# Kernel optimization log

Measured on AMD Instinct MI355X. Metric: run time of the kernel, lower is better.

Reference implementation:

```python
import jax, jax.numpy as jnp
import numpy as np
from jax import lax

B, S, D_IN, D_OUT = 2, 1024, 2048, 2048
H, DK, DV, K = 8, 64, 128, 4
CONV_DIM = H * (3 * DK + DV)  # q,k,f each DK per head; v is DV per head
G = H * DV


def _rsa_scan(q, k, v, f, W):
    # q,k,f: [B,S,H,DK]; v: [B,S,H,DV]; W: [H,DV,DV]
    # matrix-valued per-head state St: [B,H,DK,DV], GRU-style gated update
    qs = jnp.moveaxis(q, 1, 0)
    ks = jnp.moveaxis(k, 1, 0)
    vs = jnp.moveaxis(v, 1, 0)
    fs = jnp.moveaxis(f, 1, 0)
    S0 = jnp.zeros((q.shape[0], H, DK, DV), q.dtype)

    def step(St, xs):
        qt, kt, vt, ft = xs
        g = jax.nn.sigmoid(ft)  # [B,H,DK] forget gate
        cand = jnp.tanh(vt[:, :, None, :] + jnp.einsum('bhkv,hvw->bhkw', St, W))
        St = g[..., None] * St + kt[..., None] * cand  # [B,H,DK,DV]
        yt = jnp.einsum('bhk,bhkv->bhv', qt, St)  # readout [B,H,DV]
        return St, yt

    _, ys = lax.scan(step, S0, (qs, ks, vs, fs))
    return jnp.moveaxis(ys, 0, 1)  # [B,S,H,DV]


def setup_inputs() -> dict:
    key = jax.random.key(0)
    ks = jax.random.split(key, 11)
    std = 0.02
    return {
        'x': jax.random.normal(ks[0], (B, S, D_IN), jnp.float32),
        'w_in': jax.random.normal(ks[1], (CONV_DIM + G, D_IN), jnp.float32) * std,
        'b_in': jax.random.normal(ks[2], (CONV_DIM + G,), jnp.float32) * std,
        'conv_w': jax.random.normal(ks[3], (CONV_DIM, 1, K), jnp.float32) * std,
        'conv_b': jax.random.normal(ks[4], (CONV_DIM,), jnp.float32) * std,
        'D': 1.0 + 0.1 * jax.random.normal(ks[5], (H, DV), jnp.float32),
        'state_weight': jax.random.normal(ks[6], (H, DV, DV), jnp.float32) * std,
        'forget_multiplier': 0.1 * jax.random.normal(ks[7], (H,), jnp.float32),
        'forget_bias': 0.1 * jax.random.normal(ks[8], (H, DK), jnp.float32),
        'g_w': 1.0 + 0.1 * jax.random.normal(ks[9], (G,), jnp.float32),
        'w_out': jax.random.normal(ks[10], (D_OUT, G), jnp.float32) * std,
    }


def reference(x, w_in, b_in, conv_w, conv_b, D, state_weight, forget_multiplier, forget_bias, g_w, w_out):
    h = x @ w_in.T + b_in  # input projection [B,S,CONV_DIM+G]
    conv_in, gate = h[..., :CONV_DIM], h[..., CONV_DIM:]
    # causal depthwise conv1d (left pad K-1) + SiLU activation
    xc = jnp.swapaxes(conv_in, 1, 2)  # [B,C,S]
    yc = lax.conv_general_dilated(xc, conv_w, (1,), [(K - 1, 0)], feature_group_count=CONV_DIM)
    yc = jax.nn.silu(yc + conv_b[None, :, None])
    yc = jnp.swapaxes(yc, 1, 2)  # [B,S,CONV_DIM]
    o = 0
    q = yc[..., o:o + H * DK].reshape(B, S, H, DK); o += H * DK
    k = yc[..., o:o + H * DK].reshape(B, S, H, DK); o += H * DK
    v = yc[..., o:o + H * DV].reshape(B, S, H, DV); o += H * DV
    f = yc[..., o:o + H * DK].reshape(B, S, H, DK)
    # p=2 key normalization over head dim (elementwise_affine=False)
    k = k * lax.rsqrt(jnp.sum(k * k, -1, keepdims=True) + 1e-12)
    f = 2.0 * jax.nn.sigmoid(forget_multiplier)[None, None, :, None] * (f + forget_bias[None, None])
    y = _rsa_scan(q, k, v, f, state_weight)  # [B,S,H,DV]
    y = (y + v * D[None, None]).reshape(B, S, G)
    y = y * jax.nn.silu(gate)
    y = y * lax.rsqrt(jnp.mean(y * y, -1, keepdims=True) + 1e-6) * g_w  # RMSNorm
    return y @ w_out.T
```

## Files before the change

### kernel.cpp

```cpp
#include <hip/hip_runtime.h>

typedef unsigned short u16;
typedef unsigned int u32;
typedef __attribute__((ext_vector_type(8))) short short8;
typedef __attribute__((ext_vector_type(4))) float f32x4;

#define N_B 2
#define N_S 1024
#define N_DIN 2048
#define N_DOUT 2048
#define N_H 8
#define N_DK 64
#define N_DV 128
#define N_CONVD 2560
#define N_G 1024
#define N_NH 3584

#define TANH_SCALE 2.8853901817f
#define INV_TANH_SCALE 0.34657359f

__device__ __forceinline__ u16 f2bf(float f) {
  u32 u = __float_as_uint(f);
  u32 r = (u + 0x7FFFu + ((u >> 16) & 1u)) >> 16;
  return (u16)r;
}
__device__ __forceinline__ float fsigmoid(float x) {
  return __builtin_amdgcn_rcpf(1.f + __builtin_amdgcn_exp2f(-1.44269504f * x));
}
__device__ __forceinline__ u32 pack_bf16_rhu(float a, float b) {
  u32 ua = __float_as_uint(a) + 0x8000u;
  u32 ub = __float_as_uint(b) + 0x8000u;
  return __builtin_amdgcn_perm(ub, ua, 0x07060302u);
}
__device__ __forceinline__ void gll16(const void* g, void* l) {
  __builtin_amdgcn_global_load_lds((const __attribute__((address_space(1))) u32*)g,
                                   (__attribute__((address_space(3))) u32*)l, 16, 0, 0);
}

__global__ void cvt_kernel(const float* __restrict__ src, u16* __restrict__ dst, int n) {
  int i4 = (blockIdx.x * 256 + threadIdx.x) * 4;
  if (i4 + 3 < n) {
    float4 v = *(const float4*)&src[i4];
    dst[i4 + 0] = f2bf(v.x);
    dst[i4 + 1] = f2bf(v.y);
    dst[i4 + 2] = f2bf(v.z);
    dst[i4 + 3] = f2bf(v.w);
  }
}

__global__ void wtprep_kernel(const float* __restrict__ sw, u16* __restrict__ wtb) {
  int idx = blockIdx.x * 256 + threadIdx.x;
  if (idx >= N_H * 128 * 128) return;
  int h = idx >> 14;
  int rem = idx & 16383;
  int j = rem >> 7, v = rem & 127;
  wtb[idx] = f2bf(TANH_SCALE * sw[((size_t)h * 128 + v) * 128 + j]);
}

__global__ __launch_bounds__(256, 2) void gemm_bt(const u16* __restrict__ A,
                                                  const u16* __restrict__ B,
                                                  const float* __restrict__ bias,
                                                  float* __restrict__ C, int M, int N, int K) {
  const int tid = threadIdx.x;
  const int lane = tid & 63, w = tid >> 6;
  const int u = lane >> 4, m16 = lane & 15;
  const int wm = w & 1, wn = w >> 1;
  const int m0 = blockIdx.y * 128, n0 = blockIdx.x * 128;

  __shared__ __align__(16) u16 As[128 * 32];
  __shared__ __align__(16) u16 Bs[128 * 32];

  f32x4 acc[4][4];
#pragma unroll
  for (int i = 0; i < 4; ++i)
#pragma unroll
    for (int j = 0; j < 4; ++j)
#pragma unroll
      for (int r = 0; r < 4; ++r) acc[i][j][r] = 0.f;

  const int row0 = tid >> 2, col0 = (tid & 3) * 8;
  for (int kk = 0; kk < K; kk += 32) {
#pragma unroll
    for (int q = 0; q < 2; ++q) {
      int chunk = tid + 256 * q;
      int row = row0 + 64 * q;
      gll16(&A[(size_t)(m0 + row) * K + kk + col0], &As[chunk * 8]);
      gll16(&B[(size_t)(n0 + row) * K + kk + col0], &Bs[chunk * 8]);
    }
    __syncthreads();
    short8 af[4], bfr[4];
#pragma unroll
    for (int i = 0; i < 4; ++i) af[i] = *(const short8*)&As[(64 * wm + 16 * i + m16) * 32 + 8 * u];
#pragma unroll
    for (int i = 0; i < 4; ++i) bfr[i] = *(const short8*)&Bs[(64 * wn + 16 * i + m16) * 32 + 8 * u];
#pragma unroll
    for (int am = 0; am < 4; ++am)
#pragma unroll
      for (int bn = 0; bn < 4; ++bn)
        acc[am][bn] = __builtin_amdgcn_mfma_f32_16x16x32_bf16(af[am], bfr[bn], acc[am][bn], 0, 0, 0);
    __syncthreads();
  }
#pragma unroll
  for (int am = 0; am < 4; ++am)
#pragma unroll
    for (int bn = 0; bn < 4; ++bn) {
      int n = n0 + 64 * wn + 16 * bn + m16;
      float bv = bias ? bias[n] : 0.f;
#pragma unroll
      for (int r = 0; r < 4; ++r) {
        int m = m0 + 64 * wm + 16 * am + 4 * u + r;
        C[(size_t)m * N + n] = acc[am][bn][r] + bv;
      }
    }
}

__global__ __launch_bounds__(320, 4) void conv_kernel(const float* __restrict__ h,
                                                      const float* __restrict__ cw,
                                                      const float* __restrict__ cb,
                                                      const float* __restrict__ fm,
                                                      const float* __restrict__ fb,
                                                      float* __restrict__ SCIN) {
  const int bid = blockIdx.x;
  const int t = bid & 1023, chain = bid >> 10;
  const int b = chain >> 3, hh = chain & 7;
  const int tid = threadIdx.x;

  int c, outoff;
  if (tid < 64) { c = hh * 64 + tid; outoff = tid * 4; }
  else if (tid < 128) { int i = tid - 64; c = 512 + hh * 64 + i; outoff = i * 4 + 1; }
  else if (tid < 192) { int i = tid - 128; c = 2048 + hh * 64 + i; outoff = i * 4 + 2; }
  else { int j = tid - 192; c = 1024 + hh * 128 + j; outoff = 256 + j; }

  float4 w4 = *(const float4*)&cw[c * 4];
  const float* wp = (const float*)&w4;
  float acc = cb[c];
  const float* hrow = h + ((size_t)(b * 1024 + t)) * N_NH + c;
#pragma unroll
  for (int j = 0; j < 4; ++j) {
    int tt = t - 3 + j;
    if (tt >= 0) acc += wp[j] * hrow[(ptrdiff_t)(j - 3) * N_NH];
  }
  float yv = acc * fsigmoid(acc);

  if (tid >= 64 && tid < 128) {
    float s = yv * yv;
#pragma unroll
    for (int m = 1; m < 64; m <<= 1) s += __shfl_xor(s, m, 64);
    yv *= __builtin_amdgcn_rsqf(s + 1e-12f);
  } else if (tid >= 128 && tid < 192) {
    float scale2 = 2.f * fsigmoid(fm[hh]);
    yv = fsigmoid(scale2 * (yv + fb[hh * 64 + (tid - 128)]));
  } else if (tid >= 192) {
    yv *= TANH_SCALE;
  }
  SCIN[(size_t)bid * 384 + outoff] = yv;
}

__global__ __launch_bounds__(512, 2) void scan_kernel(const u16* __restrict__ Wtb,
                                                      const float* __restrict__ SCIN,
                                                      float* __restrict__ Ybp) {
  const int tid = threadIdx.x;
  const int lane = tid & 63, wv = tid >> 6;
  const int u = lane >> 4, m16 = lane & 15;
  const int chain = blockIdx.x >> 2;
  const int ig = blockIdx.x & 3;
  const int hh = chain & 7;

  __shared__ __align__(16) u16 Slds[2][16 * 136];

  short8 Wfrag[4];
  {
    const u16* wb = Wtb + ((size_t)hh * 128 + (16 * wv + m16)) * 128 + 8 * u;
#pragma unroll
    for (int kc = 0; kc < 4; ++kc) Wfrag[kc] = *(const short8*)(wb + 32 * kc);
  }

  for (int x = tid; x < 2 * 16 * 136; x += 512) ((u16*)Slds)[x] = 0;

  const float* scin_c = SCIN + (size_t)chain * 1024 * 384;
  float* ybase = Ybp + ((size_t)(chain * 4 + ig)) * 1024 * 128;

  float Sreg[4] = {0.f, 0.f, 0.f, 0.f};

  float4 qkg = *(const float4*)&scin_c[(16 * ig + m16) * 4];
  float4 v4 = *(const float4*)&scin_c[256 + 16 * wv + 4 * u];

  __syncthreads();

  for (int t = 0; t < 1024; ++t) {
    const int tn = (t + 1) & 1023;
    const float* pn = scin_c + (size_t)tn * 384;
    float4 qkgn = *(const float4*)&pn[(16 * ig + m16) * 4];
    float4 vn = *(const float4*)&pn[256 + 16 * wv + 4 * u];

    const u16* Sr = Slds[t & 1];
    u16* Sw = Slds[(t + 1) & 1];

    short8 Bfrag[4];
#pragma unroll
    for (int kc = 0; kc < 4; ++kc)
      Bfrag[kc] = *(const short8*)&Sr[m16 * 136 + 32 * kc + 8 * u];

    f32x4 acc0, acc1 = {0.f, 0.f, 0.f, 0.f};
    acc0[0] = v4.x; acc0[1] = v4.y; acc0[2] = v4.z; acc0[3] = v4.w;
    acc0 = __builtin_amdgcn_mfma_f32_16x16x32_bf16(Wfrag[0], Bfrag[0], acc0, 0, 0, 0);
    acc1 = __builtin_amdgcn_mfma_f32_16x16x32_bf16(Wfrag[1], Bfrag[1], acc1, 0, 0, 0);
    acc0 = __builtin_amdgcn_mfma_f32_16x16x32_bf16(Wfrag[2], Bfrag[2], acc0, 0, 0, 0);
    acc1 = __builtin_amdgcn_mfma_f32_16x16x32_bf16(Wfrag[3], Bfrag[3], acc1, 0, 0, 0);

    const float qv = qkg.x, kv = qkg.y, gv = qkg.z;
    float p[4];
#pragma unroll
    for (int r = 0; r < 4; ++r) {
      float arg = acc0[r] + acc1[r];
      float e = __builtin_amdgcn_exp2f(arg);
      float cand = 1.f - 2.f * __builtin_amdgcn_rcpf(e + 1.f);
      Sreg[r] = gv * Sreg[r] + kv * cand;
      p[r] = qv * Sreg[r];
    }

    uint2 pck;
    pck.x = pack_bf16_rhu(Sreg[0], Sreg[1]);
    pck.y = pack_bf16_rhu(Sreg[2], Sreg[3]);
    *(uint2*)&Sw[m16 * 136 + 16 * wv + 4 * u] = pck;

#pragma unroll
    for (int r = 0; r < 4; ++r) {
      float pr = p[r];
      pr += __int_as_float(__builtin_amdgcn_update_dpp(0, __float_as_int(pr), 0x111, 0xF, 0xF, true));
      pr += __int_as_float(__builtin_amdgcn_update_dpp(0, __float_as_int(pr), 0x112, 0xF, 0xF, true));
      pr += __int_as_float(__builtin_amdgcn_update_dpp(0, __float_as_int(pr), 0x114, 0xF, 0xF, true));
      pr += __int_as_float(__builtin_amdgcn_update_dpp(0, __float_as_int(pr), 0x118, 0xF, 0xF, true));
      p[r] = pr;
    }
    if (m16 == 15) {
      f32x4 yo;
      yo[0] = p[0]; yo[1] = p[1]; yo[2] = p[2]; yo[3] = p[3];
      *(f32x4*)(ybase + (size_t)t * 128 + 16 * wv + 4 * u) = yo;
    }

    asm volatile("s_waitcnt lgkmcnt(0)\n\ts_barrier" ::: "memory");

    qkg = qkgn; v4 = vn;
  }
}

__global__ __launch_bounds__(256, 2) void post_kernel(const float* __restrict__ Ybp,
                                                      const float* __restrict__ SCIN,
                                                      const float* __restrict__ h,
                                                      const float* __restrict__ Dp,
                                                      const float* __restrict__ gwv,
                                                      u16* __restrict__ Zb) {
  const int bt = blockIdx.x;
  const int b = bt >> 10, t = bt & 1023;
  const int lane = threadIdx.x & 63, wvi = threadIdx.x >> 6;
  float z[4];
  float ss = 0.f;
#pragma unroll
  for (int c = 0; c < 4; ++c) {
    int j = threadIdx.x + 256 * c;
    int head = j >> 7, dv = j & 127;
    int chain = b * 8 + head;
    float y = 0.f;
#pragma unroll
    for (int igx = 0; igx < 4; ++igx)
      y += Ybp[(((size_t)(chain * 4 + igx)) * 1024 + t) * 128 + dv];
    float v = SCIN[((size_t)chain * 1024 + t) * 384 + 256 + dv];
    float gate = h[((size_t)(b * 1024 + t)) * N_NH + 2560 + j];
    float zz = (y + v * (Dp[j] * INV_TANH_SCALE)) * (gate * fsigmoid(gate));
    z[c] = zz;
    ss += zz * zz;
  }
#pragma unroll
  for (int m = 1; m < 64; m <<= 1) ss += __shfl_xor(ss, m, 64);
  __shared__ float red[4];
  if (lane == 0) red[wvi] = ss;
  __syncthreads();
  float tot = red[0] + red[1] + red[2] + red[3];
  float scale = __builtin_amdgcn_rsqf(tot * (1.f / 1024.f) + 1e-6f);
#pragma unroll
  for (int c = 0; c < 4; ++c) {
    int j = threadIdx.x + 256 * c;
    Zb[(size_t)(b * 1024 + t) * 1024 + j] = f2bf(z[c] * scale * gwv[j]);
  }
}

extern "C" void kernel_launch(void* const* d_in, const int* in_sizes, int n_in,
                              void* d_out, int out_size, void* d_ws, size_t ws_size,
                              hipStream_t stream) {
  const float* x    = (const float*)d_in[0];
  const float* w_in = (const float*)d_in[1];
  const float* b_in = (const float*)d_in[2];
  const float* cw   = (const float*)d_in[3];
  const float* cb   = (const float*)d_in[4];
  const float* Dp   = (const float*)d_in[5];
  const float* sw   = (const float*)d_in[6];
  const float* fm   = (const float*)d_in[7];
  const float* fb   = (const float*)d_in[8];
  const float* gwv  = (const float*)d_in[9];
  const float* wo   = (const float*)d_in[10];
  float* out = (float*)d_out;

  char* p = (char*)d_ws;
  auto alloc = [&](size_t bytes) {
    char* r = p;
    p += (bytes + 255) & ~(size_t)255;
    return r;
  };
  u16* xb    = (u16*)alloc((size_t)2048 * 2048 * 2);
  u16* wib   = (u16*)alloc((size_t)3584 * 2048 * 2);
  u16* wob   = (u16*)alloc((size_t)2048 * 1024 * 2);
  u16* wtb   = (u16*)alloc((size_t)8 * 128 * 128 * 2);
  float* hbf = (float*)alloc((size_t)2048 * 3584 * 4);
  float* scin= (float*)alloc((size_t)16 * 1024 * 384 * 4);
  float* ybp = (float*)alloc((size_t)64 * 1024 * 128 * 4);
  u16* zb    = (u16*)alloc((size_t)2048 * 1024 * 2);

  cvt_kernel<<<4096, 256, 0, stream>>>(x, xb, 2048 * 2048);
  cvt_kernel<<<7168, 256, 0, stream>>>(w_in, wib, 3584 * 2048);
  cvt_kernel<<<2048, 256, 0, stream>>>(wo, wob, 2048 * 1024);
  wtprep_kernel<<<512, 256, 0, stream>>>(sw, wtb);

  gemm_bt<<<dim3(3584 / 128, 2048 / 128), 256, 0, stream>>>(xb, wib, b_in, hbf, 2048, 3584, 2048);

  conv_kernel<<<16 * 1024, 320, 0, stream>>>(hbf, cw, cb, fm, fb, scin);

  scan_kernel<<<64, 512, 0, stream>>>(wtb, scin, ybp);

  post_kernel<<<2048, 256, 0, stream>>>(ybp, scin, hbf, Dp, gwv, zb);

  gemm_bt<<<dim3(2048 / 128, 2048 / 128), 256, 0, stream>>>(zb, wob, nullptr, out, 2048, 2048, 1024);
}
```

Measured before the change: 663.4 us.

## Defer scan readout reduction a step and XOR-swizzle state LDS layout

Moves the per-step readout DPP reduction and output store off the recurrence critical path by computing them one iteration later, where they can overlap with the next step's MFMAs. Replaces the padded LDS state buffer with an XOR-swizzled unpadded layout to avoid bank conflicts, and issues the state reads before the global prefetch. It also folds the tanh candidate update into two FMAs. This adds a loop epilogue and live registers for the deferred partial products.

```diff
diff --git a/kernel.cpp b/kernel.cpp
--- a/kernel.cpp
+++ b/kernel.cpp
@@ -36,6 +36,13 @@
   __builtin_amdgcn_global_load_lds((const __attribute__((address_space(1))) u32*)g,
                                    (__attribute__((address_space(3))) u32*)l, 16, 0, 0);
 }
+__device__ __forceinline__ float dpp_prefix16(float x) {
+  x += __int_as_float(__builtin_amdgcn_update_dpp(0, __float_as_int(x), 0x111, 0xF, 0xF, true));
+  x += __int_as_float(__builtin_amdgcn_update_dpp(0, __float_as_int(x), 0x112, 0xF, 0xF, true));
+  x += __int_as_float(__builtin_amdgcn_update_dpp(0, __float_as_int(x), 0x114, 0xF, 0xF, true));
+  x += __int_as_float(__builtin_amdgcn_update_dpp(0, __float_as_int(x), 0x118, 0xF, 0xF, true));
+  return x;
+}
 
 __global__ void cvt_kernel(const float* __restrict__ src, u16* __restrict__ dst, int n) {
   int i4 = (blockIdx.x * 256 + threadIdx.x) * 4;
@@ -166,7 +173,7 @@
   const int ig = blockIdx.x & 3;
   const int hh = chain & 7;
 
-  __shared__ __align__(16) u16 Slds[2][16 * 136];
+  __shared__ __align__(16) u16 Slds[2][16 * 128];
 
   short8 Wfrag[4];
   {
@@ -175,31 +182,51 @@
     for (int kc = 0; kc < 4; ++kc) Wfrag[kc] = *(const short8*)(wb + 32 * kc);
   }
 
-  for (int x = tid; x < 2 * 16 * 136; x += 512) ((u16*)Slds)[x] = 0;
+  for (int x = tid; x < 2048; x += 512) ((u32*)Slds)[x] = 0u;
+
+  const int xr = m16 & 7;
+  int rdoff[4];
+#pragma unroll
+  for (int kc = 0; kc < 4; ++kc) rdoff[kc] = m16 * 256 + (((4 * kc + u) ^ xr) << 4);
+  const int wroff = m16 * 256 + ((((wv << 1) + (u >> 1)) ^ xr) << 4) + ((u & 1) << 3);
 
   const float* scin_c = SCIN + (size_t)chain * 1024 * 384;
   float* ybase = Ybp + ((size_t)(chain * 4 + ig)) * 1024 * 128;
 
   float Sreg[4] = {0.f, 0.f, 0.f, 0.f};
+  float pp[4] = {0.f, 0.f, 0.f, 0.f};
 
   float4 qkg = *(const float4*)&scin_c[(16 * ig + m16) * 4];
   float4 v4 = *(const float4*)&scin_c[256 + 16 * wv + 4 * u];
 
   __syncthreads();
 
+  char* ldsbase = (char*)&Slds[0][0];
+
   for (int t = 0; t < 1024; ++t) {
+    const char* Sr = ldsbase + ((t & 1) << 12);
+    char* Sw = ldsbase + (((t + 1) & 1) << 12);
+
+    short8 Bfrag[4];
+#pragma unroll
+    for (int kc = 0; kc < 4; ++kc) Bfrag[kc] = *(const short8*)(Sr + rdoff[kc]);
+
     const int tn = (t + 1) & 1023;
     const float* pn = scin_c + (size_t)tn * 384;
     float4 qkgn = *(const float4*)&pn[(16 * ig + m16) * 4];
     float4 vn = *(const float4*)&pn[256 + 16 * wv + 4 * u];
 
-    const u16* Sr = Slds[t & 1];
-    u16* Sw = Slds[(t + 1) & 1];
-
-    short8 Bfrag[4];
-#pragma unroll
-    for (int kc = 0; kc < 4; ++kc)
-      Bfrag[kc] = *(const short8*)&Sr[m16 * 136 + 32 * kc + 8 * u];
+    if (t > 0) {
+      float y0 = dpp_prefix16(pp[0]);
+      float y1 = dpp_prefix16(pp[1]);
+      float y2 = dpp_prefix16(pp[2]);
+      float y3 = dpp_prefix16(pp[3]);
+      if (m16 == 15) {
+        f32x4 yo;
+        yo[0] = y0; yo[1] = y1; yo[2] = y2; yo[3] = y3;
+        *(f32x4*)(ybase + (size_t)(t - 1) * 128 + 16 * wv + 4 * u) = yo;
+      }
+    }
 
     f32x4 acc0, acc1 = {0.f, 0.f, 0.f, 0.f};
     acc0[0] = v4.x; acc0[1] = v4.y; acc0[2] = v4.z; acc0[3] = v4.w;
@@ -209,39 +236,39 @@
     acc1 = __builtin_amdgcn_mfma_f32_16x16x32_bf16(Wfrag[3], Bfrag[3], acc1, 0, 0, 0);
 
     const float qv = qkg.x, kv = qkg.y, gv = qkg.z;
-    float p[4];
+    const float k2 = -2.f * kv;
 #pragma unroll
     for (int r = 0; r < 4; ++r) {
       float arg = acc0[r] + acc1[r];
       float e = __builtin_amdgcn_exp2f(arg);
-      float cand = 1.f - 2.f * __builtin_amdgcn_rcpf(e + 1.f);
-      Sreg[r] = gv * Sreg[r] + kv * cand;
-      p[r] = qv * Sreg[r];
+      float rc = __builtin_amdgcn_rcpf(e + 1.f);
+      float base = __builtin_fmaf(gv, Sreg[r], kv);
+      Sreg[r] = __builtin_fmaf(k2, rc, base);
     }
 
     uint2 pck;
     pck.x = pack_bf16_rhu(Sreg[0], Sreg[1]);
     pck.y = pack_bf16_rhu(Sreg[2], Sreg[3]);
-    *(uint2*)&Sw[m16 * 136 + 16 * wv + 4 * u] = pck;
-
-#pragma unroll
-    for (int r = 0; r < 4; ++r) {
-      float pr = p[r];
-      pr += __int_as_float(__builtin_amdgcn_update_dpp(0, __float_as_int(pr), 0x111, 0xF, 0xF, true));
-      pr += __int_as_float(__builtin_amdgcn_update_dpp(0, __float_as_int(pr), 0x112, 0xF, 0xF, true));
-      pr += __int_as_float(__builtin_amdgcn_update_dpp(0, __float_as_int(pr), 0x114, 0xF, 0xF, true));
-      pr += __int_as_float(__builtin_amdgcn_update_dpp(0, __float_as_int(pr), 0x118, 0xF, 0xF, true));
-      p[r] = pr;
-    }
+    *(uint2*)(Sw + wroff) = pck;
+
+#pragma unroll
+    for (int r = 0; r < 4; ++r) pp[r] = qv * Sreg[r];
+
+    asm volatile("s_waitcnt lgkmcnt(0)\n\ts_barrier" ::: "memory");
+
+    qkg = qkgn; v4 = vn;
+  }
+
+  {
+    float y0 = dpp_prefix16(pp[0]);
+    float y1 = dpp_prefix16(pp[1]);
+    float y2 = dpp_prefix16(pp[2]);
+    float y3 = dpp_prefix16(pp[3]);
     if (m16 == 15) {
       f32x4 yo;
-      yo[0] = p[0]; yo[1] = p[1]; yo[2] = p[2]; yo[3] = p[3];
-      *(f32x4*)(ybase + (size_t)t * 128 + 16 * wv + 4 * u) = yo;
-    }
-
-    asm volatile("s_waitcnt lgkmcnt(0)\n\ts_barrier" ::: "memory");
-
-    qkg = qkgn; v4 = vn;
+      yo[0] = y0; yo[1] = y1; yo[2] = y2; yo[3] = y3;
+      *(f32x4*)(ybase + (size_t)1023 * 128 + 16 * wv + 4 * u) = yo;
+    }
   }
 }
 
```

New measurement: 762.8 us. 1.15x slower.

## Split scan DK rows across more blocks based on available workspace

Applied to the files above, without the earlier changes.

The scan kernel is templated on how many DK rows each block owns (V). With enough workspace, 256 or 128 blocks run instead of 64, and each block loads only V distinct q/k/g rows, zeroing q for padded lanes. The per-row update is also folded into FMAs. Post_kernel then sums a variable number of partial outputs. This aims to raise parallelism on the latency-bound sequential scan, at the cost of duplicated 128x128 recurrence work, more MFMA per useful row, and more partial-output traffic in post_kernel.

```diff
diff --git a/kernel.cpp b/kernel.cpp
--- a/kernel.cpp
+++ b/kernel.cpp
@@ -36,6 +36,13 @@
   __builtin_amdgcn_global_load_lds((const __attribute__((address_space(1))) u32*)g,
                                    (__attribute__((address_space(3))) u32*)l, 16, 0, 0);
 }
+__device__ __forceinline__ float dpp_prefix16(float x) {
+  x += __int_as_float(__builtin_amdgcn_update_dpp(0, __float_as_int(x), 0x111, 0xF, 0xF, true));
+  x += __int_as_float(__builtin_amdgcn_update_dpp(0, __float_as_int(x), 0x112, 0xF, 0xF, true));
+  x += __int_as_float(__builtin_amdgcn_update_dpp(0, __float_as_int(x), 0x114, 0xF, 0xF, true));
+  x += __int_as_float(__builtin_amdgcn_update_dpp(0, __float_as_int(x), 0x118, 0xF, 0xF, true));
+  return x;
+}
 
 __global__ void cvt_kernel(const float* __restrict__ src, u16* __restrict__ dst, int n) {
   int i4 = (blockIdx.x * 256 + threadIdx.x) * 4;
@@ -156,14 +163,16 @@
   SCIN[(size_t)bid * 384 + outoff] = yv;
 }
 
+template <int V>
 __global__ __launch_bounds__(512, 2) void scan_kernel(const u16* __restrict__ Wtb,
                                                       const float* __restrict__ SCIN,
                                                       float* __restrict__ Ybp) {
+  const int NIG = 64 / V;
   const int tid = threadIdx.x;
   const int lane = tid & 63, wv = tid >> 6;
   const int u = lane >> 4, m16 = lane & 15;
-  const int chain = blockIdx.x >> 2;
-  const int ig = blockIdx.x & 3;
+  const int chain = blockIdx.x / NIG;
+  const int ig = blockIdx.x - chain * NIG;
   const int hh = chain & 7;
 
   __shared__ __align__(16) u16 Slds[2][16 * 136];
@@ -178,11 +187,15 @@
   for (int x = tid; x < 2 * 16 * 136; x += 512) ((u16*)Slds)[x] = 0;
 
   const float* scin_c = SCIN + (size_t)chain * 1024 * 384;
-  float* ybase = Ybp + ((size_t)(chain * 4 + ig)) * 1024 * 128;
+  float* ybase = Ybp + ((size_t)(chain * NIG + ig)) * 1024 * 128;
+
+  const int iload = V * ig + (m16 < V ? m16 : V - 1);
+  const bool qzero = (V < 16) && (m16 >= V);
 
   float Sreg[4] = {0.f, 0.f, 0.f, 0.f};
 
-  float4 qkg = *(const float4*)&scin_c[(16 * ig + m16) * 4];
+  float4 qkg = *(const float4*)&scin_c[iload * 4];
+  if (qzero) qkg.x = 0.f;
   float4 v4 = *(const float4*)&scin_c[256 + 16 * wv + 4 * u];
 
   __syncthreads();
@@ -190,7 +203,7 @@
   for (int t = 0; t < 1024; ++t) {
     const int tn = (t + 1) & 1023;
     const float* pn = scin_c + (size_t)tn * 384;
-    float4 qkgn = *(const float4*)&pn[(16 * ig + m16) * 4];
+    float4 qkgn = *(const float4*)&pn[iload * 4];
     float4 vn = *(const float4*)&pn[256 + 16 * wv + 4 * u];
 
     const u16* Sr = Slds[t & 1];
@@ -209,13 +222,15 @@
     acc1 = __builtin_amdgcn_mfma_f32_16x16x32_bf16(Wfrag[3], Bfrag[3], acc1, 0, 0, 0);
 
     const float qv = qkg.x, kv = qkg.y, gv = qkg.z;
+    const float k2 = -2.f * kv;
     float p[4];
 #pragma unroll
     for (int r = 0; r < 4; ++r) {
       float arg = acc0[r] + acc1[r];
       float e = __builtin_amdgcn_exp2f(arg);
-      float cand = 1.f - 2.f * __builtin_amdgcn_rcpf(e + 1.f);
-      Sreg[r] = gv * Sreg[r] + kv * cand;
+      float rc = __builtin_amdgcn_rcpf(e + 1.f);
+      float base = __builtin_fmaf(gv, Sreg[r], kv);
+      Sreg[r] = __builtin_fmaf(k2, rc, base);
       p[r] = qv * Sreg[r];
     }
 
@@ -225,14 +240,7 @@
     *(uint2*)&Sw[m16 * 136 + 16 * wv + 4 * u] = pck;
 
 #pragma unroll
-    for (int r = 0; r < 4; ++r) {
-      float pr = p[r];
-      pr += __int_as_float(__builtin_amdgcn_update_dpp(0, __float_as_int(pr), 0x111, 0xF, 0xF, true));
-      pr += __int_as_float(__builtin_amdgcn_update_dpp(0, __float_as_int(pr), 0x112, 0xF, 0xF, true));
-      pr += __int_as_float(__builtin_amdgcn_update_dpp(0, __float_as_int(pr), 0x114, 0xF, 0xF, true));
-      pr += __int_as_float(__builtin_amdgcn_update_dpp(0, __float_as_int(pr), 0x118, 0xF, 0xF, true));
-      p[r] = pr;
-    }
+    for (int r = 0; r < 4; ++r) p[r] = dpp_prefix16(p[r]);
     if (m16 == 15) {
       f32x4 yo;
       yo[0] = p[0]; yo[1] = p[1]; yo[2] = p[2]; yo[3] = p[3];
@@ -241,7 +249,9 @@
 
     asm volatile("s_waitcnt lgkmcnt(0)\n\ts_barrier" ::: "memory");
 
-    qkg = qkgn; v4 = vn;
+    qkg = qkgn;
+    if (qzero) qkg.x = 0.f;
+    v4 = vn;
   }
 }
 
@@ -250,7 +260,7 @@
                                                       const float* __restrict__ h,
                                                       const float* __restrict__ Dp,
                                                       const float* __restrict__ gwv,
-                                                      u16* __restrict__ Zb) {
+                                                      u16* __restrict__ Zb, int nparts) {
   const int bt = blockIdx.x;
   const int b = bt >> 10, t = bt & 1023;
   const int lane = threadIdx.x & 63, wvi = threadIdx.x >> 6;
@@ -262,9 +272,8 @@
     int head = j >> 7, dv = j & 127;
     int chain = b * 8 + head;
     float y = 0.f;
-#pragma unroll
-    for (int igx = 0; igx < 4; ++igx)
-      y += Ybp[(((size_t)(chain * 4 + igx)) * 1024 + t) * 128 + dv];
+    for (int igx = 0; igx < nparts; ++igx)
+      y += Ybp[(((size_t)(chain * nparts + igx)) * 1024 + t) * 128 + dv];
     float v = SCIN[((size_t)chain * 1024 + t) * 384 + 256 + dv];
     float gate = h[((size_t)(b * 1024 + t)) * N_NH + 2560 + j];
     float zz = (y + v * (Dp[j] * INV_TANH_SCALE)) * (gate * fsigmoid(gate));
@@ -313,8 +322,15 @@
   u16* wtb   = (u16*)alloc((size_t)8 * 128 * 128 * 2);
   float* hbf = (float*)alloc((size_t)2048 * 3584 * 4);
   float* scin= (float*)alloc((size_t)16 * 1024 * 384 * 4);
-  float* ybp = (float*)alloc((size_t)64 * 1024 * 128 * 4);
   u16* zb    = (u16*)alloc((size_t)2048 * 1024 * 2);
+
+  size_t used = (size_t)(p - (char*)d_ws);
+  size_t avail = (ws_size > used) ? ws_size - used : 0;
+  const size_t per_part = (size_t)16 * 1024 * 128 * 4;
+  int nig = 4;
+  if (avail >= 16 * per_part) nig = 16;
+  else if (avail >= 8 * per_part) nig = 8;
+  float* ybp = (float*)alloc((size_t)nig * per_part);
 
   cvt_kernel<<<4096, 256, 0, stream>>>(x, xb, 2048 * 2048);
   cvt_kernel<<<7168, 256, 0, stream>>>(w_in, wib, 3584 * 2048);
@@ -325,9 +341,11 @@
 
   conv_kernel<<<16 * 1024, 320, 0, stream>>>(hbf, cw, cb, fm, fb, scin);
 
-  scan_kernel<<<64, 512, 0, stream>>>(wtb, scin, ybp);
-
-  post_kernel<<<2048, 256, 0, stream>>>(ybp, scin, hbf, Dp, gwv, zb);
+  if (nig == 16)      scan_kernel<4><<<16 * 16, 512, 0, stream>>>(wtb, scin, ybp);
+  else if (nig == 8)  scan_kernel<8><<<16 * 8, 512, 0, stream>>>(wtb, scin, ybp);
+  else                scan_kernel<16><<<16 * 4, 512, 0, stream>>>(wtb, scin, ybp);
+
+  post_kernel<<<2048, 256, 0, stream>>>(ybp, scin, hbf, Dp, gwv, zb, nig);
 
   gemm_bt<<<dim3(2048 / 128, 2048 / 128), 256, 0, stream>>>(zb, wob, nullptr, out, 2048, 2048, 1024);
 }
```

Result: slower. 703.3 us (+6.0%).

## Restructure scan so each 4-wave block handles two key-row groups

Applied to the files above, without the earlier changes.

The scan kernel now runs 32 blocks of 256 threads instead of 64 blocks of 512. Each block processes two 16-row key groups of a chain, and each wave owns 32 output columns using two W fragments. Barrier cost is shared across twice the work, and the two independent MFMA chains interleave to hide latency. In exchange, each wave runs a longer serial instruction sequence per timestep and only half as many CUs are used. The tanh update is also folded into fused FMAs.

```diff
diff --git a/kernel.cpp b/kernel.cpp
--- a/kernel.cpp
+++ b/kernel.cpp
@@ -36,6 +36,13 @@
   __builtin_amdgcn_global_load_lds((const __attribute__((address_space(1))) u32*)g,
                                    (__attribute__((address_space(3))) u32*)l, 16, 0, 0);
 }
+__device__ __forceinline__ float dpp_prefix16(float x) {
+  x += __int_as_float(__builtin_amdgcn_update_dpp(0, __float_as_int(x), 0x111, 0xF, 0xF, true));
+  x += __int_as_float(__builtin_amdgcn_update_dpp(0, __float_as_int(x), 0x112, 0xF, 0xF, true));
+  x += __int_as_float(__builtin_amdgcn_update_dpp(0, __float_as_int(x), 0x114, 0xF, 0xF, true));
+  x += __int_as_float(__builtin_amdgcn_update_dpp(0, __float_as_int(x), 0x118, 0xF, 0xF, true));
+  return x;
+}
 
 __global__ void cvt_kernel(const float* __restrict__ src, u16* __restrict__ dst, int n) {
   int i4 = (blockIdx.x * 256 + threadIdx.x) * 4;
@@ -156,92 +163,144 @@
   SCIN[(size_t)bid * 384 + outoff] = yv;
 }
 
-__global__ __launch_bounds__(512, 2) void scan_kernel(const u16* __restrict__ Wtb,
+__global__ __launch_bounds__(256, 1) void scan_kernel(const u16* __restrict__ Wtb,
                                                       const float* __restrict__ SCIN,
                                                       float* __restrict__ Ybp) {
   const int tid = threadIdx.x;
   const int lane = tid & 63, wv = tid >> 6;
   const int u = lane >> 4, m16 = lane & 15;
-  const int chain = blockIdx.x >> 2;
-  const int ig = blockIdx.x & 3;
+  const int chain = blockIdx.x >> 1;
+  const int pair = blockIdx.x & 1;
+  const int igA = 2 * pair, igB = 2 * pair + 1;
   const int hh = chain & 7;
 
-  __shared__ __align__(16) u16 Slds[2][16 * 136];
-
-  short8 Wfrag[4];
-  {
-    const u16* wb = Wtb + ((size_t)hh * 128 + (16 * wv + m16)) * 128 + 8 * u;
-#pragma unroll
-    for (int kc = 0; kc < 4; ++kc) Wfrag[kc] = *(const short8*)(wb + 32 * kc);
-  }
-
-  for (int x = tid; x < 2 * 16 * 136; x += 512) ((u16*)Slds)[x] = 0;
+  __shared__ __align__(16) u16 Slds[2][2][16 * 136];
+
+  short8 Wfrag[2][4];
+#pragma unroll
+  for (int s = 0; s < 2; ++s) {
+    const u16* wb = Wtb + ((size_t)hh * 128 + (32 * wv + 16 * s + m16)) * 128 + 8 * u;
+#pragma unroll
+    for (int kc = 0; kc < 4; ++kc) Wfrag[s][kc] = *(const short8*)(wb + 32 * kc);
+  }
+
+  for (int x = tid; x < 4352; x += 256) ((u32*)Slds)[x] = 0u;
 
   const float* scin_c = SCIN + (size_t)chain * 1024 * 384;
-  float* ybase = Ybp + ((size_t)(chain * 4 + ig)) * 1024 * 128;
-
-  float Sreg[4] = {0.f, 0.f, 0.f, 0.f};
-
-  float4 qkg = *(const float4*)&scin_c[(16 * ig + m16) * 4];
-  float4 v4 = *(const float4*)&scin_c[256 + 16 * wv + 4 * u];
+  float* ybA = Ybp + ((size_t)(chain * 4 + igA)) * 1024 * 128;
+  float* ybB = Ybp + ((size_t)(chain * 4 + igB)) * 1024 * 128;
+
+  f32x4 SA[2], SB[2];
+#pragma unroll
+  for (int s = 0; s < 2; ++s)
+#pragma unroll
+    for (int r = 0; r < 4; ++r) { SA[s][r] = 0.f; SB[s][r] = 0.f; }
+
+  float4 qA = *(const float4*)&scin_c[(16 * igA + m16) * 4];
+  float4 qB = *(const float4*)&scin_c[(16 * igB + m16) * 4];
+  float4 v0 = *(const float4*)&scin_c[256 + 32 * wv + 4 * u];
+  float4 v1 = *(const float4*)&scin_c[256 + 32 * wv + 16 + 4 * u];
 
   __syncthreads();
 
+  const int rdo = m16 * 136 + 8 * u;
+  const int wro0 = m16 * 136 + 32 * wv + 4 * u;
+
   for (int t = 0; t < 1024; ++t) {
-    const int tn = (t + 1) & 1023;
-    const float* pn = scin_c + (size_t)tn * 384;
-    float4 qkgn = *(const float4*)&pn[(16 * ig + m16) * 4];
-    float4 vn = *(const float4*)&pn[256 + 16 * wv + 4 * u];
-
-    const u16* Sr = Slds[t & 1];
-    u16* Sw = Slds[(t + 1) & 1];
-
-    short8 Bfrag[4];
-#pragma unroll
-    for (int kc = 0; kc < 4; ++kc)
-      Bfrag[kc] = *(const short8*)&Sr[m16 * 136 + 32 * kc + 8 * u];
-
-    f32x4 acc0, acc1 = {0.f, 0.f, 0.f, 0.f};
-    acc0[0] = v4.x; acc0[1] = v4.y; acc0[2] = v4.z; acc0[3] = v4.w;
-    acc0 = __builtin_amdgcn_mfma_f32_16x16x32_bf16(Wfrag[0], Bfrag[0], acc0, 0, 0, 0);
-    acc1 = __builtin_amdgcn_mfma_f32_16x16x32_bf16(Wfrag[1], Bfrag[1], acc1, 0, 0, 0);
-    acc0 = __builtin_amdgcn_mfma_f32_16x16x32_bf16(Wfrag[2], Bfrag[2], acc0, 0, 0, 0);
-    acc1 = __builtin_amdgcn_mfma_f32_16x16x32_bf16(Wfrag[3], Bfrag[3], acc1, 0, 0, 0);
-
-    const float qv = qkg.x, kv = qkg.y, gv = qkg.z;
-    float p[4];
-#pragma unroll
-    for (int r = 0; r < 4; ++r) {
-      float arg = acc0[r] + acc1[r];
-      float e = __builtin_amdgcn_exp2f(arg);
-      float cand = 1.f - 2.f * __builtin_amdgcn_rcpf(e + 1.f);
-      Sreg[r] = gv * Sreg[r] + kv * cand;
-      p[r] = qv * Sreg[r];
+    const u16* SrA = Slds[0][t & 1];
+    u16* SwA = Slds[0][(t + 1) & 1];
+    const u16* SrB = Slds[1][t & 1];
+    u16* SwB = Slds[1][(t + 1) & 1];
+
+    short8 Ba[4], Bb[4];
+#pragma unroll
+    for (int kc = 0; kc < 4; ++kc) Ba[kc] = *(const short8*)&SrA[rdo + 32 * kc];
+#pragma unroll
+    for (int kc = 0; kc < 4; ++kc) Bb[kc] = *(const short8*)&SrB[rdo + 32 * kc];
+
+    const float* pn = scin_c + (size_t)((t + 1) & 1023) * 384;
+    float4 qAn = *(const float4*)&pn[(16 * igA + m16) * 4];
+    float4 qBn = *(const float4*)&pn[(16 * igB + m16) * 4];
+    float4 v0n = *(const float4*)&pn[256 + 32 * wv + 4 * u];
+    float4 v1n = *(const float4*)&pn[256 + 32 * wv + 16 + 4 * u];
+
+    f32x4 a0, a1;
+    a0[0] = v0.x; a0[1] = v0.y; a0[2] = v0.z; a0[3] = v0.w;
+    a1[0] = v1.x; a1[1] = v1.y; a1[2] = v1.z; a1[3] = v1.w;
+#pragma unroll
+    for (int kc = 0; kc < 4; ++kc) a0 = __builtin_amdgcn_mfma_f32_16x16x32_bf16(Wfrag[0][kc], Ba[kc], a0, 0, 0, 0);
+#pragma unroll
+    for (int kc = 0; kc < 4; ++kc) a1 = __builtin_amdgcn_mfma_f32_16x16x32_bf16(Wfrag[1][kc], Ba[kc], a1, 0, 0, 0);
+    {
+      const float qv = qA.x, kv = qA.y, gv = qA.z, k2 = -2.f * kv;
+      float p0[4], p1[4];
+#pragma unroll
+      for (int r = 0; r < 4; ++r) {
+        float e0 = __builtin_amdgcn_exp2f(a0[r]);
+        float rc0 = __builtin_amdgcn_rcpf(e0 + 1.f);
+        SA[0][r] = __builtin_fmaf(k2, rc0, __builtin_fmaf(gv, SA[0][r], kv));
+        p0[r] = qv * SA[0][r];
+        float e1 = __builtin_amdgcn_exp2f(a1[r]);
+        float rc1 = __builtin_amdgcn_rcpf(e1 + 1.f);
+        SA[1][r] = __builtin_fmaf(k2, rc1, __builtin_fmaf(gv, SA[1][r], kv));
+        p1[r] = qv * SA[1][r];
+      }
+      uint2 w0, w1;
+      w0.x = pack_bf16_rhu(SA[0][0], SA[0][1]); w0.y = pack_bf16_rhu(SA[0][2], SA[0][3]);
+      w1.x = pack_bf16_rhu(SA[1][0], SA[1][1]); w1.y = pack_bf16_rhu(SA[1][2], SA[1][3]);
+      *(uint2*)&SwA[wro0] = w0;
+      *(uint2*)&SwA[wro0 + 16] = w1;
+#pragma unroll
+      for (int r = 0; r < 4; ++r) { p0[r] = dpp_prefix16(p0[r]); p1[r] = dpp_prefix16(p1[r]); }
+      if (m16 == 15) {
+        f32x4 y0, y1;
+#pragma unroll
+        for (int r = 0; r < 4; ++r) { y0[r] = p0[r]; y1[r] = p1[r]; }
+        *(f32x4*)(ybA + (size_t)t * 128 + 32 * wv + 4 * u) = y0;
+        *(f32x4*)(ybA + (size_t)t * 128 + 32 * wv + 16 + 4 * u) = y1;
+      }
     }
 
-    uint2 pck;
-    pck.x = pack_bf16_rhu(Sreg[0], Sreg[1]);
-    pck.y = pack_bf16_rhu(Sreg[2], Sreg[3]);
-    *(uint2*)&Sw[m16 * 136 + 16 * wv + 4 * u] = pck;
-
-#pragma unroll
-    for (int r = 0; r < 4; ++r) {
-      float pr = p[r];
-      pr += __int_as_float(__builtin_amdgcn_update_dpp(0, __float_as_int(pr), 0x111, 0xF, 0xF, true));
-      pr += __int_as_float(__builtin_amdgcn_update_dpp(0, __float_as_int(pr), 0x112, 0xF, 0xF, true));
-      pr += __int_as_float(__builtin_amdgcn_update_dpp(0, __float_as_int(pr), 0x114, 0xF, 0xF, true));
-      pr += __int_as_float(__builtin_amdgcn_update_dpp(0, __float_as_int(pr), 0x118, 0xF, 0xF, true));
-      p[r] = pr;
+    f32x4 b0, b1;
+    b0[0] = v0.x; b0[1] = v0.y; b0[2] = v0.z; b0[3] = v0.w;
+    b1[0] = v1.x; b1[1] = v1.y; b1[2] = v1.z; b1[3] = v1.w;
+#pragma unroll
+    for (int kc = 0; kc < 4; ++kc) b0 = __builtin_amdgcn_mfma_f32_16x16x32_bf16(Wfrag[0][kc], Bb[kc], b0, 0, 0, 0);
+#pragma unroll
+    for (int kc = 0; kc < 4; ++kc) b1 = __builtin_amdgcn_mfma_f32_16x16x32_bf16(Wfrag[1][kc], Bb[kc], b1, 0, 0, 0);
+    {
+      const float qv = qB.x, kv = qB.y, gv = qB.z, k2 = -2.f * kv;
+      float p0[4], p1[4];
+#pragma unroll
+      for (int r = 0; r < 4; ++r) {
+        float e0 = __builtin_amdgcn_exp2f(b0[r]);
+        float rc0 = __builtin_amdgcn_rcpf(e0 + 1.f);
+        SB[0][r] = __builtin_fmaf(k2, rc0, __builtin_fmaf(gv, SB[0][r], kv));
+        p0[r] = qv * SB[0][r];
+        float e1 = __builtin_amdgcn_exp2f(b1[r]);
+        float rc1 = __builtin_amdgcn_rcpf(e1 + 1.f);
+        SB[1][r] = __builtin_fmaf(k2, rc1, __builtin_fmaf(gv, SB[1][r], kv));
+        p1[r] = qv * SB[1][r];
+      }
+      uint2 w0, w1;
+      w0.x = pack_bf16_rhu(SB[0][0], SB[0][1]); w0.y = pack_bf16_rhu(SB[0][2], SB[0][3]);
+      w1.x = pack_bf16_rhu(SB[1][0], SB[1][1]); w1.y = pack_bf16_rhu(SB[1][2], SB[1][3]);
+      *(uint2*)&SwB[wro0] = w0;
+      *(uint2*)&SwB[wro0 + 16] = w1;
+#pragma unroll
+      for (int r = 0; r < 4; ++r) { p0[r] = dpp_prefix16(p0[r]); p1[r] = dpp_prefix16(p1[r]); }
+      if (m16 == 15) {
+        f32x4 y0, y1;
+#pragma unroll
+        for (int r = 0; r < 4; ++r) { y0[r] = p0[r]; y1[r] = p1[r]; }
+        *(f32x4*)(ybB + (size_t)t * 128 + 32 * wv + 4 * u) = y0;
+        *(f32x4*)(ybB + (size_t)t * 128 + 32 * wv + 16 + 4 * u) = y1;
+      }
     }
-    if (m16 == 15) {
-      f32x4 yo;
-      yo[0] = p[0]; yo[1] = p[1]; yo[2] = p[2]; yo[3] = p[3];
-      *(f32x4*)(ybase + (size_t)t * 128 + 16 * wv + 4 * u) = yo;
-    }
 
     asm volatile("s_waitcnt lgkmcnt(0)\n\ts_barrier" ::: "memory");
 
-    qkg = qkgn; v4 = vn;
+    qA = qAn; qB = qBn; v0 = v0n; v1 = v1n;
   }
 }
 
@@ -325,7 +384,7 @@
 
   conv_kernel<<<16 * 1024, 320, 0, stream>>>(hbf, cw, cb, fm, fb, scin);
 
-  scan_kernel<<<64, 512, 0, stream>>>(wtb, scin, ybp);
+  scan_kernel<<<32, 256, 0, stream>>>(wtb, scin, ybp);
 
   post_kernel<<<2048, 256, 0, stream>>>(ybp, scin, hbf, Dp, gwv, zb);
 
```

After: 1.098 ms. 1.65x slower.
